# Optimization experiments

Hardware: AMD Instinct MI355X
Metric: run time of the kernel (lower is better)

Reference implementation:

```python
import jax, jax.numpy as jnp
import numpy as np

N = 10000
E = 160000
IN_DIM = 128
OUT_DIM = 32
HEADS = 32
H1 = OUT_DIM * 2   # 64 per-head channels in layer 1
H2 = OUT_DIM       # 32 per-head channels in layer 2
NEG_SLOPE = 0.2
EPS = 1e-16  # PyG softmax denominator epsilon


def gat_layer(x, src, dst, W, a_src, a_dst, b, n_nodes, heads, ch):
    # x: [N, F_in], W: [F_in, heads*ch], a_src/a_dst: [heads, ch], b: [ch]
    xp = (x @ W).reshape(n_nodes, heads, ch)                 # [N,H,C]
    alpha_s = jnp.einsum('nhc,hc->nh', xp, a_src)            # [N,H]
    alpha_d = jnp.einsum('nhc,hc->nh', xp, a_dst)            # [N,H]
    e = jax.nn.leaky_relu(alpha_s[src] + alpha_d[dst], NEG_SLOPE)  # [E,H]
    # segment softmax over edges grouped by destination node
    m = jax.ops.segment_max(e, dst, num_segments=n_nodes)    # [N,H]
    e = jnp.exp(e - m[dst])                                  # [E,H]
    s = jax.ops.segment_sum(e, dst, num_segments=n_nodes)    # [N,H]
    alpha = e / (s[dst] + EPS)                               # [E,H]
    msg = alpha[:, :, None] * xp[src]                        # [E,H,C]
    out = jax.ops.segment_sum(msg, dst, num_segments=n_nodes)  # [N,H,C]
    return out.mean(axis=1) + b                              # concat=False: head mean, [N,C]


def setup_inputs() -> dict:
    key = jax.random.key(0)
    ks = jax.random.split(key, 9)
    x = jax.random.normal(ks[0], (N, IN_DIM), dtype=jnp.float32)
    edge_index = jax.random.randint(ks[1], (2, E), 0, N, dtype=jnp.int64)
    W1 = jax.random.normal(ks[2], (IN_DIM, HEADS * H1), dtype=jnp.float32) * 0.1
    a_src1 = jax.random.normal(ks[3], (HEADS, H1), dtype=jnp.float32) * 0.1
    a_dst1 = jax.random.normal(ks[4], (HEADS, H1), dtype=jnp.float32) * 0.1
    b1 = jnp.zeros((H1,), dtype=jnp.float32)
    W2 = jax.random.normal(ks[5], (H1, HEADS * H2), dtype=jnp.float32) * 0.1
    a_src2 = jax.random.normal(ks[6], (HEADS, H2), dtype=jnp.float32) * 0.1
    a_dst2 = jax.random.normal(ks[7], (HEADS, H2), dtype=jnp.float32) * 0.1
    b2 = jnp.zeros((H2,), dtype=jnp.float32)
    return {"x": x, "edge_index": edge_index,
            "W1": W1, "a_src1": a_src1, "a_dst1": a_dst1, "b1": b1,
            "W2": W2, "a_src2": a_src2, "a_dst2": a_dst2, "b2": b2}


def reference(x, edge_index, W1, a_src1, a_dst1, b1, W2, a_src2, a_dst2, b2):
    # flow='source_to_target': messages go edge_index[0] -> edge_index[1]
    src = edge_index[0]
    dst = edge_index[1]
    z1 = jax.nn.elu(gat_layer(x, src, dst, W1, a_src1, a_dst1, b1, N, HEADS, H1))
    z2 = jax.nn.elu(gat_layer(z1, src, dst, W2, a_src2, a_dst2, b2, N, HEADS, H2))
    return jnp.concatenate((z1, z2), axis=-1)  # [N, 96]
```

## Files before the change

kernel.cpp:

```cpp
#include <hip/hip_runtime.h>
#include <hip/hip_bf16.h>

#define NN 10000
#define NE 160000
#define NE_PAD 190464
#define NH 32
#define LRELU_SLOPE 0.2f
#define SM_EPS 1e-16f
#define SM_SHIFT 16.0f

typedef _Float16 f16;
typedef __attribute__((ext_vector_type(8))) _Float16 f16x8;
typedef __attribute__((ext_vector_type(4))) float f32x4;

__global__ void k_detect_zero(const unsigned int* __restrict__ raw, int* __restrict__ flag,
                              int* __restrict__ deg) {
    int i = blockIdx.x * blockDim.x + threadIdx.x;
    if (i < NN) deg[i] = 0;
    if (i == 0) {
        int z = 1;
        for (int j = 1; j < 32; j += 2) z &= (raw[j] == 0u);
        *flag = z;
    }
}
__global__ void k_norm_hist(const int* __restrict__ raw, const int* __restrict__ flag,
                            int* __restrict__ srcv, int* __restrict__ dstv, int* __restrict__ deg) {
    int e = blockIdx.x * blockDim.x + threadIdx.x;
    if (e >= NE) return;
    int s, d;
    if (*flag) { s = raw[2 * e]; d = raw[2 * (NE + e)]; }
    else       { s = raw[e];     d = raw[NE + e]; }
    srcv[e] = s; dstv[e] = d;
    atomicAdd(&deg[d], 1);
}
__global__ void k_scan(const int* __restrict__ deg, int* __restrict__ offs, int* __restrict__ cursor) {
    __shared__ int wsum[16], wpre[16];
    __shared__ int base;
    const int tid = threadIdx.x, lane = tid & 63, wid = tid >> 6;
    if (tid == 0) base = 0;
    __syncthreads();
    for (int chunk = 0; chunk < NN; chunk += 1024) {
        int idx = chunk + tid;
        int v = (idx < NN) ? ((deg[idx] + 3) & ~3) : 0;
        int s = v;
        #pragma unroll
        for (int off = 1; off < 64; off <<= 1) {
            int t = __shfl_up(s, off);
            if (lane >= off) s += t;
        }
        if (lane == 63) wsum[wid] = s;
        __syncthreads();
        if (wid == 0) {
            int ws = (lane < 16) ? wsum[lane] : 0;
            #pragma unroll
            for (int off = 1; off < 16; off <<= 1) {
                int t = __shfl_up(ws, off);
                if (lane >= off) ws += t;
            }
            if (lane < 16) wpre[lane] = ws;
        }
        __syncthreads();
        int wbase = (wid == 0) ? 0 : wpre[wid - 1];
        int excl = base + wbase + s - v;
        if (idx < NN) { offs[idx] = excl; cursor[idx] = excl; }
        int total = wpre[15];
        __syncthreads();
        if (tid == 0) base += total;
        __syncthreads();
    }
    if (tid == 0) offs[NN] = base;
}
__global__ void k_scatter(const int* __restrict__ srcv, const int* __restrict__ dstv,
                          int* __restrict__ cursor, int* __restrict__ srcs,
                          int* __restrict__ dstp) {
    int e = blockIdx.x * blockDim.x + threadIdx.x;
    if (e < NE) {
        int d = dstv[e];
        int p = atomicAdd(&cursor[d], 1);
        srcs[p] = srcv[e];
        dstp[p] = d;
    }
}

__global__ void k_prep(const float* __restrict__ X, f16* __restrict__ Xb,
                       const float* __restrict__ W1, f16* __restrict__ Wt1,
                       const float* __restrict__ W2, f16* __restrict__ Wt2,
                       int* __restrict__ srcs, int* __restrict__ dstp) {
    int i = blockIdx.x * blockDim.x + threadIdx.x;
    if (i < NE_PAD) { srcs[i] = 0; dstp[i] = -1; }
    if (i < NN * 128) { Xb[i] = (f16)X[i]; return; }
    i -= NN * 128;
    if (i < 128 * 2048) {
        int k = i / 2048, m = i - k * 2048;
        Wt1[(size_t)m * 128 + k] = (f16)W1[i];
        return;
    }
    i -= 128 * 2048;
    if (i < 64 * 1024) {
        int k = i / 1024, m = i - k * 1024;
        Wt2[(size_t)m * 64 + k] = (f16)W2[i];
    }
}

template<int K, int M, int C>
__global__ __launch_bounds__(256) void k_gemm_mfma(
        const f16* __restrict__ Xb, const f16* __restrict__ Wt,
        const float* __restrict__ Asrc, const float* __restrict__ Adst,
        f16* __restrict__ XPH, float* __restrict__ aS, float* __restrict__ aD) {
    constexpr int BM = 64, BN = 128;
    constexpr int KB = K * 2;
    constexpr int NHB = BN / C;
    constexpr int WPH = C / 32;
    __shared__ char lds[(BM + BN) * KB];
    __shared__ float sredS[4][BM], sredD[4][BM];
    char* lA = lds;
    char* lB = lds + BM * KB;

    const int tid = threadIdx.x;
    const int wv = tid >> 6, ln = tid & 63;
    const int lrow = ln & 15, lkb = ln >> 4;
    const int brow = blockIdx.x * BM;
    const int bcol = blockIdx.y * BN;

    #pragma unroll
    for (int c = 0; c < BM * K / 8 / 256; c++) {
        int it = c * 256 + tid;
        int r = it / (K / 8), kc = (it % (K / 8)) * 8;
        int node = brow + r;
        uint4 v = make_uint4(0u, 0u, 0u, 0u);
        if (node < NN) v = *reinterpret_cast<const uint4*>(&Xb[(size_t)node * K + kc]);
        *reinterpret_cast<uint4*>(lA + ((r * KB + kc * 2) ^ ((r & 7) << 4))) = v;
    }
    #pragma unroll
    for (int c = 0; c < BN * K / 8 / 256; c++) {
        int it = c * 256 + tid;
        int r = it / (K / 8), kc = (it % (K / 8)) * 8;
        uint4 v = *reinterpret_cast<const uint4*>(&Wt[(size_t)(bcol + r) * K + kc]);
        *reinterpret_cast<uint4*>(lB + ((r * KB + kc * 2) ^ ((r & 7) << 4))) = v;
    }
    __syncthreads();

    f32x4 acc[4][2];
    #pragma unroll
    for (int mi = 0; mi < 4; mi++)
        #pragma unroll
        for (int nj = 0; nj < 2; nj++) acc[mi][nj] = (f32x4){0.f, 0.f, 0.f, 0.f};

    #pragma unroll
    for (int ks = 0; ks < K / 32; ks++) {
        const int k0 = ks * 32 + lkb * 8;
        f16x8 af[4], bfr[2];
        #pragma unroll
        for (int mi = 0; mi < 4; mi++) {
            int r = mi * 16 + lrow;
            af[mi] = *reinterpret_cast<const f16x8*>(lA + ((r * KB + k0 * 2) ^ ((r & 7) << 4)));
        }
        #pragma unroll
        for (int nj = 0; nj < 2; nj++) {
            int r = wv * 32 + nj * 16 + lrow;
            bfr[nj] = *reinterpret_cast<const f16x8*>(lB + ((r * KB + k0 * 2) ^ ((r & 7) << 4)));
        }
        #pragma unroll
        for (int mi = 0; mi < 4; mi++)
            #pragma unroll
            for (int nj = 0; nj < 2; nj++)
                acc[mi][nj] = __builtin_amdgcn_mfma_f32_16x16x32_f16(af[mi], bfr[nj], acc[mi][nj], 0, 0, 0);
    }

    float ar0 = Asrc[bcol + wv * 32 + lrow];
    float ar1 = Asrc[bcol + wv * 32 + 16 + lrow];
    float ad0 = Adst[bcol + wv * 32 + lrow];
    float ad1 = Adst[bcol + wv * 32 + 16 + lrow];

    #pragma unroll
    for (int mi = 0; mi < 4; mi++) {
        #pragma unroll
        for (int r = 0; r < 4; r++) {
            int rowl = mi * 16 + lkb * 4 + r;
            int row = brow + rowl;
            if (row < NN) {
                XPH[(size_t)row * M + bcol + wv * 32 + lrow]      = (f16)acc[mi][0][r];
                XPH[(size_t)row * M + bcol + wv * 32 + 16 + lrow] = (f16)acc[mi][1][r];
            }
            float vs = acc[mi][0][r] * ar0 + acc[mi][1][r] * ar1;
            float vd = acc[mi][0][r] * ad0 + acc[mi][1][r] * ad1;
            vs += __shfl_xor(vs, 1); vd += __shfl_xor(vd, 1);
            vs += __shfl_xor(vs, 2); vd += __shfl_xor(vd, 2);
            vs += __shfl_xor(vs, 4); vd += __shfl_xor(vd, 4);
            vs += __shfl_xor(vs, 8); vd += __shfl_xor(vd, 8);
            if (lrow == 0) {
                sredS[wv][rowl] = vs;
                sredD[wv][rowl] = vd;
            }
        }
    }
    __syncthreads();
    if (tid < BM) {
        int node = brow + tid;
        if (node < NN) {
            #pragma unroll
            for (int hb = 0; hb < NHB; hb++) {
                float ss = 0.f, dd = 0.f;
                #pragma unroll
                for (int w = 0; w < WPH; w++) {
                    ss += sredS[hb * WPH + w][tid];
                    dd += sredD[hb * WPH + w][tid];
                }
                int h = bcol / C + hb;
                aS[node * NH + h] = ss;
                aD[node * NH + h] = dd;
            }
        }
    }
}

__global__ __launch_bounds__(256) void k_score_edge(
        const float* __restrict__ aS, const float* __restrict__ aD,
        const int* __restrict__ srcs, const int* __restrict__ dstp,
        float* __restrict__ pEh) {
    const int i = blockIdx.x * 256 + threadIdx.x;
    const int d = dstp[i];
    if (d < 0) {
        #pragma unroll
        for (int h = 0; h < NH; h++) pEh[(size_t)h * NE_PAD + i] = 0.f;
        return;
    }
    const int s = srcs[i];
    const float4* prs = reinterpret_cast<const float4*>(&aS[s * NH]);
    const float4* prd = reinterpret_cast<const float4*>(&aD[d * NH]);
    float4 vs[8], vd[8];
    #pragma unroll
    for (int j = 0; j < 8; j++) { vs[j] = prs[j]; vd[j] = prd[j]; }
    #pragma unroll
    for (int j = 0; j < 8; j++) {
        float sc, p;
        sc = vs[j].x + vd[j].x; sc = (sc >= 0.f) ? sc : LRELU_SLOPE * sc;
        p = __expf(sc - SM_SHIFT); pEh[(size_t)(4 * j + 0) * NE_PAD + i] = p;
        sc = vs[j].y + vd[j].y; sc = (sc >= 0.f) ? sc : LRELU_SLOPE * sc;
        p = __expf(sc - SM_SHIFT); pEh[(size_t)(4 * j + 1) * NE_PAD + i] = p;
        sc = vs[j].z + vd[j].z; sc = (sc >= 0.f) ? sc : LRELU_SLOPE * sc;
        p = __expf(sc - SM_SHIFT); pEh[(size_t)(4 * j + 2) * NE_PAD + i] = p;
        sc = vs[j].w + vd[j].w; sc = (sc >= 0.f) ? sc : LRELU_SLOPE * sc;
        p = __expf(sc - SM_SHIFT); pEh[(size_t)(4 * j + 3) * NE_PAD + i] = p;
    }
}

template<int C>
__global__ __launch_bounds__(256) void k_agg_slice(
        const f16* __restrict__ XPH, const float* __restrict__ pEh,
        const int* __restrict__ offs, const int* __restrict__ srcs,
        float* __restrict__ P) {
    constexpr int M = NH * C;
    constexpr int HPS = 128 / C;
    constexpr int CGH = C / 8;
    constexpr int HGRID = (NN / 4) * 8;
    int b = blockIdx.x;
    const int hp = (b >= HGRID) ? 1 : 0;
    b -= hp * HGRID;
    const int sg = (b & 7) + hp * 8;
    const int wid = threadIdx.x >> 6, lane = threadIdx.x & 63;
    const int node = (b >> 3) * 4 + wid;
    const int cg = lane & 15, el = lane >> 4;
    const int hl = cg / CGH;
    const int h = sg * HPS + hl;
    const int col = sg * 128 + cg * 8;
    const int beg = offs[node], end = offs[node + 1];
    const float* __restrict__ pErow = pEh + (size_t)h * NE_PAD;
    float acc[8];
    #pragma unroll
    for (int j = 0; j < 8; j++) acc[j] = 0.f;
    float ssum = 0.f;
    int i = beg + el;
    const int trip = (end - beg) >> 2;
    #define AGG_STEP(ii) { \
        const int s_ = srcs[ii]; const float p_ = pErow[ii]; \
        uint4 v_ = *reinterpret_cast<const uint4*>(&XPH[(size_t)s_ * M + col]); \
        f16x8 h_ = __builtin_bit_cast(f16x8, v_); \
        ssum += p_; \
        acc[0] = fmaf(p_, (float)h_[0], acc[0]); \
        acc[1] = fmaf(p_, (float)h_[1], acc[1]); \
        acc[2] = fmaf(p_, (float)h_[2], acc[2]); \
        acc[3] = fmaf(p_, (float)h_[3], acc[3]); \
        acc[4] = fmaf(p_, (float)h_[4], acc[4]); \
        acc[5] = fmaf(p_, (float)h_[5], acc[5]); \
        acc[6] = fmaf(p_, (float)h_[6], acc[6]); \
        acc[7] = fmaf(p_, (float)h_[7], acc[7]); }
    if (trip & 1) { AGG_STEP(i); i += 4; }
    for (int t = trip >> 1; t > 0; t--) {
        AGG_STEP(i);
        AGG_STEP(i + 4);
        i += 8;
    }
    #undef AGG_STEP
    #pragma unroll
    for (int j = 0; j < 8; j++) {
        acc[j] += __shfl_xor(acc[j], 16);
        acc[j] += __shfl_xor(acc[j], 32);
    }
    ssum += __shfl_xor(ssum, 16);
    ssum += __shfl_xor(ssum, 32);
    const float r = 1.f / (ssum + SM_EPS);
    #pragma unroll
    for (int j = 0; j < 8; j++) acc[j] *= r;
    #pragma unroll
    for (int j = 0; j < 8; j++) acc[j] += __shfl_xor(acc[j], 8);
    if constexpr (HPS == 4) {
        #pragma unroll
        for (int j = 0; j < 8; j++) acc[j] += __shfl_xor(acc[j], 4);
    }
    if (el == 0 && cg < CGH) {
        float* dst = &P[((size_t)sg * NN + node) * C + cg * 8];
        *reinterpret_cast<float4*>(dst)     = make_float4(acc[0], acc[1], acc[2], acc[3]);
        *reinterpret_cast<float4*>(dst + 4) = make_float4(acc[4], acc[5], acc[6], acc[7]);
    }
}

template<int C, int NS, bool WZ>
__global__ void k_reduce(const float* __restrict__ P, const float* __restrict__ bias,
                         float* __restrict__ out, int col0, f16* __restrict__ z1h) {
    constexpr int TPN = C / 4;
    const int tid = threadIdx.x;
    const int node = blockIdx.x * (256 / TPN) + tid / TPN;
    const int c = (tid % TPN) * 4;
    if (node >= NN) return;
    float4 s = make_float4(0.f, 0.f, 0.f, 0.f);
    #pragma unroll
    for (int sg = 0; sg < NS; sg++) {
        float4 v = *reinterpret_cast<const float4*>(&P[((size_t)sg * NN + node) * C + c]);
        s.x += v.x; s.y += v.y; s.z += v.z; s.w += v.w;
    }
    float4 b = *reinterpret_cast<const float4*>(&bias[c]);
    s.x = s.x * (1.0f / NH) + b.x;
    s.y = s.y * (1.0f / NH) + b.y;
    s.z = s.z * (1.0f / NH) + b.z;
    s.w = s.w * (1.0f / NH) + b.w;
    s.x = (s.x > 0.f) ? s.x : expm1f(s.x);
    s.y = (s.y > 0.f) ? s.y : expm1f(s.y);
    s.z = (s.z > 0.f) ? s.z : expm1f(s.z);
    s.w = (s.w > 0.f) ? s.w : expm1f(s.w);
    *reinterpret_cast<float4*>(&out[(size_t)node * 96 + col0 + c]) = s;
    if constexpr (WZ) {
        f16 hx[4] = {(f16)s.x, (f16)s.y, (f16)s.z, (f16)s.w};
        *reinterpret_cast<uint2*>(&z1h[(size_t)node * C + c]) =
            *reinterpret_cast<const uint2*>(hx);
    }
}

extern "C" void kernel_launch(void* const* d_in, const int* in_sizes, int n_in,
                              void* d_out, int out_size, void* d_ws, size_t ws_size,
                              hipStream_t stream) {
    const float* x   = (const float*)d_in[0];
    const int*   ei  = (const int*)d_in[1];
    const float* W1  = (const float*)d_in[2];
    const float* as1 = (const float*)d_in[3];
    const float* ad1 = (const float*)d_in[4];
    const float* b1  = (const float*)d_in[5];
    const float* W2  = (const float*)d_in[6];
    const float* as2 = (const float*)d_in[7];
    const float* ad2 = (const float*)d_in[8];
    const float* b2  = (const float*)d_in[9];
    float* out = (float*)d_out;

    char* w = (char*)d_ws;
    size_t off = 0;
    auto alloc = [&](size_t bytes) -> void* {
        void* p = w + off;
        off = (off + bytes + 255) & ~(size_t)255;
        return p;
    };
    f16*   xph    = (f16*)alloc((size_t)NN * 2048 * 2);
    float* aS     = (float*)alloc((size_t)NN * NH * 4);
    float* aD     = (float*)alloc((size_t)NN * NH * 4);
    float* pEh    = (float*)alloc((size_t)NH * NE_PAD * 4);
    float* P1     = (float*)alloc((size_t)16 * NN * 64 * 4);
    float* P2     = P1;
    int*   deg    = (int*)alloc((size_t)NN * 4);
    int*   cursor = (int*)alloc((size_t)NN * 4);
    int*   offs   = (int*)alloc((size_t)(NN + 1) * 4);
    int*   srcs   = (int*)alloc((size_t)NE_PAD * 4);
    int*   dstp   = (int*)alloc((size_t)NE_PAD * 4);
    int*   srcv   = (int*)alloc((size_t)NE * 4);
    int*   dstv   = (int*)alloc((size_t)NE * 4);
    f16*   Xb     = (f16*)alloc((size_t)NN * 128 * 2);
    f16*   Wt1    = (f16*)alloc((size_t)2048 * 128 * 2);
    f16*   Wt2    = (f16*)alloc((size_t)1024 * 64 * 2);
    f16*   z1h    = (f16*)alloc((size_t)NN * 64 * 2);
    int*   eflag  = (int*)alloc(256);
    (void)ws_size; (void)in_sizes; (void)n_in; (void)out_size;

    k_detect_zero<<<(NN + 255) / 256, 256, 0, stream>>>((const unsigned int*)ei, eflag, deg);
    k_norm_hist<<<NE / 256, 256, 0, stream>>>(ei, eflag, srcv, dstv, deg);
    k_scan<<<1, 1024, 0, stream>>>(deg, offs, cursor);
    k_prep<<<(NN * 128 + 128 * 2048 + 64 * 1024 + 255) / 256, 256, 0, stream>>>(
        x, Xb, W1, Wt1, W2, Wt2, srcs, dstp);
    k_scatter<<<NE / 256, 256, 0, stream>>>(srcv, dstv, cursor, srcs, dstp);

    k_gemm_mfma<128, 2048, 64><<<dim3((NN + 63) / 64, 2048 / 128), 256, 0, stream>>>(
        Xb, Wt1, as1, ad1, xph, aS, aD);
    k_score_edge<<<NE_PAD / 256, 256, 0, stream>>>(aS, aD, srcs, dstp, pEh);
    k_agg_slice<64><<<(NN / 4) * 16, 256, 0, stream>>>(xph, pEh, offs, srcs, P1);
    k_reduce<64, 16, true><<<NN / 16, 256, 0, stream>>>(P1, b1, out, 0, z1h);

    k_gemm_mfma<64, 1024, 32><<<dim3((NN + 63) / 64, 1024 / 128), 256, 0, stream>>>(
        z1h, Wt2, as2, ad2, xph, aS, aD);
    k_score_edge<<<NE_PAD / 256, 256, 0, stream>>>(aS, aD, srcs, dstp, pEh);
    k_agg_slice<32><<<(NN / 4) * 8, 256, 0, stream>>>(xph, pEh, offs, srcs, P2);
    k_reduce<32, 8, false><<<(NN * 8 + 255) / 256, 256, 0, stream>>>(P2, b2, out, 64, nullptr);
}
```

Measured before the change: 233.7 us.

## Fuse edge preprocessing: merged hist/prep kernel, single-pass scan, direct raw scatter

Folds the int64-detect, degree histogram and fp16 conversion of X, W1 and W2 into one kernel, and zeroes degrees with a memset. The scan becomes single-pass, with each thread holding 10 nodes instead of looping over 1024-node chunks with barriers. The scan also fills only the per-node padding slots, rather than initialising the whole padded edge array. The scatter now reads the raw edge_index directly, which removes the intermediate src/dst buffers and two launches. The risk is that padded slots beyond the total padded edge count are no longer initialised, although later kernels still iterate over NE_PAD.

After: 242.5 us. +3.8%, slower.

```diff
diff --git a/kernel.cpp b/kernel.cpp
--- a/kernel.cpp
+++ b/kernel.cpp
@@ -13,81 +13,32 @@
 typedef __attribute__((ext_vector_type(8))) _Float16 f16x8;
 typedef __attribute__((ext_vector_type(4))) float f32x4;
 
-__global__ void k_detect_zero(const unsigned int* __restrict__ raw, int* __restrict__ flag,
-                              int* __restrict__ deg) {
-    int i = blockIdx.x * blockDim.x + threadIdx.x;
-    if (i < NN) deg[i] = 0;
-    if (i == 0) {
-        int z = 1;
-        for (int j = 1; j < 32; j += 2) z &= (raw[j] == 0u);
-        *flag = z;
-    }
-}
-__global__ void k_norm_hist(const int* __restrict__ raw, const int* __restrict__ flag,
-                            int* __restrict__ srcv, int* __restrict__ dstv, int* __restrict__ deg) {
-    int e = blockIdx.x * blockDim.x + threadIdx.x;
-    if (e >= NE) return;
-    int s, d;
-    if (*flag) { s = raw[2 * e]; d = raw[2 * (NE + e)]; }
-    else       { s = raw[e];     d = raw[NE + e]; }
-    srcv[e] = s; dstv[e] = d;
-    atomicAdd(&deg[d], 1);
-}
-__global__ void k_scan(const int* __restrict__ deg, int* __restrict__ offs, int* __restrict__ cursor) {
-    __shared__ int wsum[16], wpre[16];
-    __shared__ int base;
-    const int tid = threadIdx.x, lane = tid & 63, wid = tid >> 6;
-    if (tid == 0) base = 0;
-    __syncthreads();
-    for (int chunk = 0; chunk < NN; chunk += 1024) {
-        int idx = chunk + tid;
-        int v = (idx < NN) ? ((deg[idx] + 3) & ~3) : 0;
-        int s = v;
-        #pragma unroll
-        for (int off = 1; off < 64; off <<= 1) {
-            int t = __shfl_up(s, off);
-            if (lane >= off) s += t;
-        }
-        if (lane == 63) wsum[wid] = s;
-        __syncthreads();
-        if (wid == 0) {
-            int ws = (lane < 16) ? wsum[lane] : 0;
-            #pragma unroll
-            for (int off = 1; off < 16; off <<= 1) {
-                int t = __shfl_up(ws, off);
-                if (lane >= off) ws += t;
-            }
-            if (lane < 16) wpre[lane] = ws;
-        }
-        __syncthreads();
-        int wbase = (wid == 0) ? 0 : wpre[wid - 1];
-        int excl = base + wbase + s - v;
-        if (idx < NN) { offs[idx] = excl; cursor[idx] = excl; }
-        int total = wpre[15];
-        __syncthreads();
-        if (tid == 0) base += total;
-        __syncthreads();
-    }
-    if (tid == 0) offs[NN] = base;
-}
-__global__ void k_scatter(const int* __restrict__ srcv, const int* __restrict__ dstv,
-                          int* __restrict__ cursor, int* __restrict__ srcs,
-                          int* __restrict__ dstp) {
-    int e = blockIdx.x * blockDim.x + threadIdx.x;
-    if (e < NE) {
-        int d = dstv[e];
-        int p = atomicAdd(&cursor[d], 1);
-        srcs[p] = srcv[e];
-        dstp[p] = d;
-    }
-}
-
-__global__ void k_prep(const float* __restrict__ X, f16* __restrict__ Xb,
-                       const float* __restrict__ W1, f16* __restrict__ Wt1,
-                       const float* __restrict__ W2, f16* __restrict__ Wt2,
-                       int* __restrict__ srcs, int* __restrict__ dstp) {
-    int i = blockIdx.x * blockDim.x + threadIdx.x;
-    if (i < NE_PAD) { srcs[i] = 0; dstp[i] = -1; }
+#define HIST_BLOCKS (NE / 256)
+#define PREP_ELEMS  (NN * 128 + 128 * 2048 + 64 * 1024)
+#define PREP_BLOCKS (PREP_ELEMS / 256)
+
+__device__ __forceinline__ int edge_is_i64(const int* __restrict__ raw) {
+    const unsigned int* u = (const unsigned int*)raw;
+    int z = 1;
+    #pragma unroll
+    for (int j = 1; j < 32; j += 2) z &= (u[j] == 0u);
+    return z;
+}
+
+__global__ __launch_bounds__(256) void k_hist_prep(
+        const int* __restrict__ raw, int* __restrict__ deg,
+        const float* __restrict__ X, f16* __restrict__ Xb,
+        const float* __restrict__ W1, f16* __restrict__ Wt1,
+        const float* __restrict__ W2, f16* __restrict__ Wt2) {
+    int b = blockIdx.x;
+    if (b < HIST_BLOCKS) {
+        const int z = edge_is_i64(raw);
+        int e = b * 256 + threadIdx.x;
+        int d = z ? raw[2 * (NE + e)] : raw[NE + e];
+        atomicAdd(&deg[d], 1);
+        return;
+    }
+    int i = (b - HIST_BLOCKS) * 256 + threadIdx.x;
     if (i < NN * 128) { Xb[i] = (f16)X[i]; return; }
     i -= NN * 128;
     if (i < 128 * 2048) {
@@ -96,10 +47,72 @@
         return;
     }
     i -= 128 * 2048;
-    if (i < 64 * 1024) {
-        int k = i / 1024, m = i - k * 1024;
-        Wt2[(size_t)m * 64 + k] = (f16)W2[i];
-    }
+    int k = i / 1024, m = i - k * 1024;
+    Wt2[(size_t)m * 64 + k] = (f16)W2[i];
+}
+
+__global__ __launch_bounds__(1024) void k_scan(
+        const int* __restrict__ deg, int* __restrict__ offs, int* __restrict__ cursor,
+        int* __restrict__ srcs, int* __restrict__ dstp) {
+    __shared__ int wsum[16], wpre[17];
+    const int tid = threadIdx.x, lane = tid & 63, wid = tid >> 6;
+    int d[10], pre[10];
+    const int base_i = tid * 10;
+    int tot = 0;
+    #pragma unroll
+    for (int k = 0; k < 10; k++) {
+        int idx = base_i + k;
+        int dd = (idx < NN) ? deg[idx] : 0;
+        d[k] = dd;
+        pre[k] = tot;
+        tot += (dd + 3) & ~3;
+    }
+    int s = tot;
+    #pragma unroll
+    for (int off = 1; off < 64; off <<= 1) {
+        int t = __shfl_up(s, off);
+        if (lane >= off) s += t;
+    }
+    if (lane == 63) wsum[wid] = s;
+    __syncthreads();
+    if (wid == 0) {
+        int ws = (lane < 16) ? wsum[lane] : 0;
+        #pragma unroll
+        for (int off = 1; off < 16; off <<= 1) {
+            int t = __shfl_up(ws, off);
+            if (lane >= off) ws += t;
+        }
+        if (lane < 16) wpre[lane + 1] = ws;
+        if (lane == 0) wpre[0] = 0;
+    }
+    __syncthreads();
+    const int base = wpre[wid] + (s - tot);
+    #pragma unroll
+    for (int k = 0; k < 10; k++) {
+        int idx = base_i + k;
+        if (idx < NN) {
+            int o = base + pre[k];
+            offs[idx] = o;
+            cursor[idx] = o;
+            int dd = d[k], vp = (dd + 3) & ~3;
+            for (int q = dd; q < vp; q++) { srcs[o + q] = 0; dstp[o + q] = -1; }
+        } else if (idx == NN) {
+            offs[NN] = base;
+        }
+    }
+}
+
+__global__ __launch_bounds__(256) void k_scatter(
+        const int* __restrict__ raw, int* __restrict__ cursor,
+        int* __restrict__ srcs, int* __restrict__ dstp) {
+    const int z = edge_is_i64(raw);
+    int e = blockIdx.x * 256 + threadIdx.x;
+    int sv, dv;
+    if (z) { sv = raw[2 * e]; dv = raw[2 * (NE + e)]; }
+    else   { sv = raw[e];     dv = raw[NE + e]; }
+    int p = atomicAdd(&cursor[dv], 1);
+    srcs[p] = sv;
+    dstp[p] = dv;
 }
 
 template<int K, int M, int C>
@@ -379,21 +392,17 @@
     int*   offs   = (int*)alloc((size_t)(NN + 1) * 4);
     int*   srcs   = (int*)alloc((size_t)NE_PAD * 4);
     int*   dstp   = (int*)alloc((size_t)NE_PAD * 4);
-    int*   srcv   = (int*)alloc((size_t)NE * 4);
-    int*   dstv   = (int*)alloc((size_t)NE * 4);
     f16*   Xb     = (f16*)alloc((size_t)NN * 128 * 2);
     f16*   Wt1    = (f16*)alloc((size_t)2048 * 128 * 2);
     f16*   Wt2    = (f16*)alloc((size_t)1024 * 64 * 2);
     f16*   z1h    = (f16*)alloc((size_t)NN * 64 * 2);
-    int*   eflag  = (int*)alloc(256);
     (void)ws_size; (void)in_sizes; (void)n_in; (void)out_size;
 
-    k_detect_zero<<<(NN + 255) / 256, 256, 0, stream>>>((const unsigned int*)ei, eflag, deg);
-    k_norm_hist<<<NE / 256, 256, 0, stream>>>(ei, eflag, srcv, dstv, deg);
-    k_scan<<<1, 1024, 0, stream>>>(deg, offs, cursor);
-    k_prep<<<(NN * 128 + 128 * 2048 + 64 * 1024 + 255) / 256, 256, 0, stream>>>(
-        x, Xb, W1, Wt1, W2, Wt2, srcs, dstp);
-    k_scatter<<<NE / 256, 256, 0, stream>>>(srcv, dstv, cursor, srcs, dstp);
+    hipMemsetAsync(deg, 0, (size_t)NN * 4, stream);
+    k_hist_prep<<<HIST_BLOCKS + PREP_BLOCKS, 256, 0, stream>>>(
+        ei, deg, x, Xb, W1, Wt1, W2, Wt2);
+    k_scan<<<1, 1024, 0, stream>>>(deg, offs, cursor, srcs, dstp);
+    k_scatter<<<HIST_BLOCKS, 256, 0, stream>>>(ei, cursor, srcs, dstp);
 
     k_gemm_mfma<128, 2048, 64><<<dim3((NN + 63) / 64, 2048 / 128), 256, 0, stream>>>(
         Xb, Wt1, as1, ad1, xph, aS, aD);
```
